# Kernel tuning notes

Hardware: AMD Instinct MI355X
Metric: run time of the kernel (lower is better)

The kernel has to match this reference:

```python
import jax, jax.numpy as jnp
import numpy as np

N_NODES = 100000
N_EDGES = 1600000
N_GRAPHS = 2048
F_IN = 33
D = 256


def _graph_conv(x, edge_index, w_rel, b_rel, w_root):
    # PyG GraphConv (aggr='add'): out = lin_rel(sum_j x_j) + lin_root(x)
    src, dst = edge_index[0], edge_index[1]
    agg = jax.ops.segment_sum(x[src], dst, num_segments=x.shape[0])  # [N, F]
    return agg @ w_rel + b_rel + x @ w_root


def setup_inputs() -> dict:
    key = jax.random.key(0)
    ks = jax.random.split(key, 16)
    scale_in = 1.0 / np.sqrt(F_IN)
    scale_d = 1.0 / np.sqrt(D)
    inp = {
        "x": jax.random.normal(ks[0], (N_NODES, F_IN), dtype=jnp.float32),
        "edge_index": jax.random.randint(ks[1], (2, N_EDGES), 0, N_NODES),
        "batch_index": jnp.sort(jax.random.randint(ks[2], (N_NODES,), 0, N_GRAPHS)),
        # initial_conv: GraphConv(F_IN -> D)
        "w_rel0": jax.random.normal(ks[3], (F_IN, D), dtype=jnp.float32) * scale_in,
        "b_rel0": jnp.zeros((D,), dtype=jnp.float32),
        "w_root0": jax.random.normal(ks[4], (F_IN, D), dtype=jnp.float32) * scale_in,
        # conv1..conv3: GraphConv(D -> D)
        "w_rel1": jax.random.normal(ks[5], (D, D), dtype=jnp.float32) * scale_d,
        "b_rel1": jnp.zeros((D,), dtype=jnp.float32),
        "w_root1": jax.random.normal(ks[6], (D, D), dtype=jnp.float32) * scale_d,
        "w_rel2": jax.random.normal(ks[7], (D, D), dtype=jnp.float32) * scale_d,
        "b_rel2": jnp.zeros((D,), dtype=jnp.float32),
        "w_root2": jax.random.normal(ks[8], (D, D), dtype=jnp.float32) * scale_d,
        "w_rel3": jax.random.normal(ks[9], (D, D), dtype=jnp.float32) * scale_d,
        "b_rel3": jnp.zeros((D,), dtype=jnp.float32),
        "w_root3": jax.random.normal(ks[10], (D, D), dtype=jnp.float32) * scale_d,
        # output head Linear(D -> 1)
        "w_out": jax.random.normal(ks[11], (D, 1), dtype=jnp.float32) * scale_d,
        "b_out": jnp.zeros((1,), dtype=jnp.float32),
    }
    return inp


def reference(x, edge_index, batch_index,
              w_rel0, b_rel0, w_root0,
              w_rel1, b_rel1, w_root1,
              w_rel2, b_rel2, w_root2,
              w_rel3, b_rel3, w_root3,
              w_out, b_out):
    # dropout omitted (eval mode)
    h = jax.nn.gelu(_graph_conv(x, edge_index, w_rel0, b_rel0, w_root0))
    h = jax.nn.gelu(_graph_conv(h, edge_index, w_rel1, b_rel1, w_root1))
    h = jax.nn.gelu(_graph_conv(h, edge_index, w_rel2, b_rel2, w_root2))
    h = jax.nn.gelu(_graph_conv(h, edge_index, w_rel3, b_rel3, w_root3))
    # global mean pool over graphs
    sums = jax.ops.segment_sum(h, batch_index, num_segments=N_GRAPHS)          # [G, D]
    counts = jax.ops.segment_sum(jnp.ones((h.shape[0],), h.dtype), batch_index,
                                 num_segments=N_GRAPHS)                         # [G]
    pooled = sums / jnp.maximum(counts, 1.0)[:, None]
    return pooled @ w_out + b_out                                               # [G, 1]
```

## Files before the change

kernel.cpp:

```cpp
#include <hip/hip_runtime.h>
#include <math.h>

#define NN 100000
#define NE 1600000
#define NG 2048
#define FIN 33
#define DD 256

#define SH 8
#define NB ((NN + 255) >> 8)
#define CH 4096
#define PCAP 4608
#define ESCAP 6144

#define RBLKS ((NN + 255) / 256)

typedef __attribute__((ext_vector_type(8))) short bf16x8;
typedef __attribute__((ext_vector_type(4))) float f32x4;

__device__ __forceinline__ float b2f(unsigned short u){
    union { unsigned int i; float f; } c; c.i = ((unsigned int)u) << 16; return c.f;
}
__device__ __forceinline__ unsigned short f2b(float f){
    union { float f; unsigned int u; } c; c.f = f;
    unsigned int r = c.u + 0x7fffu + ((c.u >> 16) & 1u);
    return (unsigned short)(r >> 16);
}

__device__ __forceinline__ float gelu_tanh(float x){
    float x3 = x * x * x;
    float t = tanhf(0.7978845608028654f * (x + 0.044715f * x3));
    return 0.5f * x * (1.0f + t);
}

__global__ __launch_bounds__(256) void k_bin(const int* __restrict__ src,
                                             const int* __restrict__ dst,
                                             int* __restrict__ gcur,
                                             int2* __restrict__ pairs){
    __shared__ int cnt[NB];
    __shared__ int lb[NB];
    __shared__ int gbase[NB];
    __shared__ int sc[512];
    __shared__ int2 stage[CH];

    int t = threadIdx.x;
    for(int i = t; i < NB; i += 256) cnt[i] = 0;
    __syncthreads();

    int e0 = blockIdx.x * CH;
    int n = NE - e0; if(n > CH) n = CH;

    int  myb[16];
    int  myr[16];
    int2 myp[16];
    #pragma unroll
    for(int k = 0; k < 16; k++){
        int e = e0 + t + k * 256;
        if(e < NE){
            int s = src[e], d = dst[e];
            int b = d >> SH;
            myr[k] = atomicAdd(&cnt[b], 1);
            myb[k] = b;
            myp[k] = make_int2(s, d);
        } else myb[k] = -1;
    }
    __syncthreads();

    sc[t]       = (t       < NB) ? cnt[t]       : 0;
    sc[t + 256] = (t + 256 < NB) ? cnt[t + 256] : 0;
    __syncthreads();
    for(int off = 1; off < 512; off <<= 1){
        int a  = (t >= off)       ? sc[t - off]       : 0;
        int b2 = (t + 256 >= off) ? sc[t + 256 - off] : 0;
        __syncthreads();
        sc[t] += a; sc[t + 256] += b2;
        __syncthreads();
    }
    for(int i = t; i < NB; i += 256){
        lb[i] = sc[i] - cnt[i];
        int c = cnt[i];
        gbase[i] = (c > 0) ? atomicAdd(&gcur[i], c) : 0;
    }
    __syncthreads();

    #pragma unroll
    for(int k = 0; k < 16; k++){
        if(myb[k] >= 0) stage[lb[myb[k]] + myr[k]] = myp[k];
    }
    __syncthreads();

    for(int i = t; i < n; i += 256){
        int2 p = stage[i];
        int b = p.y >> SH;
        int tgt = gbase[b] + (i - lb[b]);
        if(tgt < PCAP) pairs[(size_t)b * PCAP + tgt] = p;
    }
}

__global__ void k_sscan(const int* __restrict__ gcur, int* __restrict__ boff){
    __shared__ int s[512];
    int t = threadIdx.x;
    int v = 0;
    if(t < NB){ v = gcur[t]; if(v > PCAP) v = PCAP; }
    s[t] = v; __syncthreads();
    for(int off = 1; off < 512; off <<= 1){
        int u = (t >= off) ? s[t - off] : 0;
        __syncthreads();
        s[t] += u;
        __syncthreads();
    }
    if(t < NB) boff[t] = s[t] - v;
}

__global__ __launch_bounds__(256) void k_bcsr(const int2* __restrict__ pairs,
                                              const int* __restrict__ gcur,
                                              const int* __restrict__ boff,
                                              int* __restrict__ deg,
                                              int* __restrict__ rs,
                                              int* __restrict__ esrc){
    __shared__ int hist[256];
    __shared__ int sc[256];
    __shared__ int cur2[256];
    __shared__ int est[ESCAP];

    int b = blockIdx.x;
    int t = threadIdx.x;
    int m = gcur[b]; if(m > PCAP) m = PCAP;
    int pstart = boff[b];
    const int2* bp = pairs + (size_t)b * PCAP;

    hist[t] = 0;
    __syncthreads();
    for(int i = t; i < m; i += 256) atomicAdd(&hist[bp[i].y & 255], 1);
    __syncthreads();

    sc[t] = hist[t]; __syncthreads();
    for(int off = 1; off < 256; off <<= 1){
        int u = (t >= off) ? sc[t - off] : 0;
        __syncthreads();
        sc[t] += u;
        __syncthreads();
    }
    int excl = sc[t] - hist[t];
    cur2[t] = excl;
    int node = (b << 8) + t;
    if(node < NN){
        deg[node] = hist[t];
        rs[node]  = pstart + excl;
    }
    __syncthreads();

    for(int i = t; i < m; i += 256){
        int2 p = bp[i];
        int pos = atomicAdd(&cur2[p.y & 255], 1);
        if(pos < ESCAP) est[pos] = p.x;
        else esrc[pstart + pos] = p.x;
    }
    __syncthreads();
    int lim = (m < ESCAP) ? m : ESCAP;
    for(int i = t; i < lim; i += 256) esrc[pstart + i] = est[i];
}

__global__ void k_xpad(const float* __restrict__ x, unsigned short* __restrict__ xb){
    int idx = blockIdx.x * 256 + threadIdx.x;
    if(idx >= NN * 64) return;
    int n = idx >> 6, c = idx & 63;
    xb[idx] = (c < FIN) ? f2b(x[(size_t)n * FIN + c]) : 0;
}

__global__ void k_aggx(const unsigned short* __restrict__ xb, const int* __restrict__ rs,
                       const int* __restrict__ deg, const int* __restrict__ esrc,
                       unsigned short* __restrict__ axb){
    int wv = (blockIdx.x * blockDim.x + threadIdx.x) >> 6;
    int lane = threadIdx.x & 63;
    int node = wv * 4 + (lane >> 4);
    int l16 = lane & 15;
    if(node >= NN) return;
    int start = rs[node], cnt = deg[node];
    float a0 = 0.f, a1 = 0.f, a2 = 0.f, a3 = 0.f;
    const unsigned short* xp = xb + l16 * 4;
    int j = 0;
    for(; j + 4 <= cnt; j += 4){
        int e0 = esrc[start+j], e1 = esrc[start+j+1], e2 = esrc[start+j+2], e3 = esrc[start+j+3];
        ushort4 v0 = *(const ushort4*)(xp + (size_t)e0 * 64);
        ushort4 v1 = *(const ushort4*)(xp + (size_t)e1 * 64);
        ushort4 v2 = *(const ushort4*)(xp + (size_t)e2 * 64);
        ushort4 v3 = *(const ushort4*)(xp + (size_t)e3 * 64);
        a0 += (b2f(v0.x) + b2f(v1.x)) + (b2f(v2.x) + b2f(v3.x));
        a1 += (b2f(v0.y) + b2f(v1.y)) + (b2f(v2.y) + b2f(v3.y));
        a2 += (b2f(v0.z) + b2f(v1.z)) + (b2f(v2.z) + b2f(v3.z));
        a3 += (b2f(v0.w) + b2f(v1.w)) + (b2f(v2.w) + b2f(v3.w));
    }
    for(; j < cnt; j++){
        int e = esrc[start + j];
        ushort4 v = *(const ushort4*)(xp + (size_t)e * 64);
        a0 += b2f(v.x); a1 += b2f(v.y); a2 += b2f(v.z); a3 += b2f(v.w);
    }
    ushort4 o; o.x = f2b(a0); o.y = f2b(a1); o.z = f2b(a2); o.w = f2b(a3);
    *(ushort4*)(axb + (size_t)node * 64 + l16 * 4) = o;
}

__global__ void k_agg256(const unsigned short* __restrict__ h, const int* __restrict__ rs,
                         const int* __restrict__ deg, const int* __restrict__ esrc,
                         unsigned short* __restrict__ agg){
    int wv = (blockIdx.x * blockDim.x + threadIdx.x) >> 6;
    int lane = threadIdx.x & 63;
    int node = wv * 2 + (lane >> 5);
    int l32 = lane & 31;
    if(node >= NN) return;
    int start = rs[node], cnt = deg[node];
    float a[8] = {0.f,0.f,0.f,0.f,0.f,0.f,0.f,0.f};
    const unsigned short* hp = h + l32 * 8;
    int j = 0;
    for(; j + 8 <= cnt; j += 8){
        bf16x8 v[8];
        #pragma unroll
        for(int q = 0; q < 8; q++){
            int e = esrc[start + j + q];
            v[q] = *(const bf16x8*)(hp + (size_t)e * DD);
        }
        #pragma unroll
        for(int q = 0; q < 8; q++)
            #pragma unroll
            for(int d = 0; d < 8; d++)
                a[d] += b2f((unsigned short)v[q][d]);
    }
    for(; j < cnt; j++){
        int e = esrc[start + j];
        bf16x8 v = *(const bf16x8*)(hp + (size_t)e * DD);
        #pragma unroll
        for(int d = 0; d < 8; d++) a[d] += b2f((unsigned short)v[d]);
    }
    bf16x8 o;
    #pragma unroll
    for(int d = 0; d < 8; d++) o[d] = (short)f2b(a[d]);
    *(bf16x8*)(agg + (size_t)node * DD + l32 * 8) = o;
}

struct WPtrs { const float* w[6]; };

__global__ void k_wt6(WPtrs wp, unsigned short* __restrict__ btAll){
    __shared__ float s[16][17];
    const float* W = wp.w[blockIdx.z];
    unsigned short* Bt = btAll + (size_t)blockIdx.z * DD * DD;
    int tx = threadIdx.x, ty = threadIdx.y;
    int k = blockIdx.y * 16 + ty;
    int j = blockIdx.x * 16 + tx;
    s[ty][tx] = W[k * DD + j];
    __syncthreads();
    Bt[(size_t)(blockIdx.x * 16 + ty) * DD + blockIdx.y * 16 + tx] = f2b(s[tx][ty]);
}

struct W2Ptrs { const float* w[2]; };

__global__ void k_wt0(W2Ptrs wp, unsigned short* __restrict__ btAll){
    int idx = blockIdx.x * 256 + threadIdx.x;
    if(idx >= DD * 64) return;
    const float* W = wp.w[blockIdx.z];
    unsigned short* Bt = btAll + (size_t)blockIdx.z * DD * 64;
    int j = idx >> 6, k = idx & 63;
    Bt[idx] = (k < FIN) ? f2b(W[(size_t)k * DD + j]) : 0;
}

template<int KS, int AST>
__global__ __launch_bounds__(512, 4) void k_mfma_gemm(
    const unsigned short* __restrict__ A0, const unsigned short* __restrict__ A1,
    const unsigned short* __restrict__ Bt0, const unsigned short* __restrict__ Bt1,
    const float* __restrict__ bias, unsigned short* __restrict__ out)
{
    constexpr int CK  = KS * 32;
    constexpr int BST = CK + 8;
    constexpr int SEG = CK / 8;
    __shared__ unsigned short Bs[128 * BST];

    int t = threadIdx.x;
    int lane = t & 63;
    int w = t >> 6;
    int r16 = lane & 15;
    int kg  = lane >> 4;

    int bid = blockIdx.x;
    int rblk = (bid >> 4) * 8 + (bid & 7);
    int chalf = (bid >> 3) & 1;
    if(rblk >= RBLKS) return;
    int i0 = rblk * 256;
    int jbase = chalf * 128;
    int baseRow = i0 + w * 32;

    f32x4 acc[2][8];
    #pragma unroll
    for(int m = 0; m < 2; m++)
        #pragma unroll
        for(int n = 0; n < 8; n++)
            acc[m][n] = (f32x4){0.f, 0.f, 0.f, 0.f};

    auto loadA = [&](int gks, bf16x8* af){
        const unsigned short* Ap = (gks < KS) ? A0 : A1;
        int kk = ((gks < KS) ? gks : gks - KS) * 32 + kg * 8;
        #pragma unroll
        for(int m = 0; m < 2; m++){
            int gi = baseRow + m * 16 + r16;
            if(gi > NN - 1) gi = NN - 1;
            af[m] = *(const bf16x8*)(Ap + (size_t)gi * AST + kk);
        }
    };

    bf16x8 afb[2][2];
    loadA(0, afb[0]);
    loadA(1, afb[1]);

    #pragma unroll
    for(int c = 0; c < 2; c++){
        const unsigned short* Bp = c ? Bt1 : Bt0;
        if(c) __syncthreads();
        #pragma unroll
        for(int p = 0; p < (128 * SEG) / 512; p++){
            int idx = p * 512 + t;
            int row = idx / SEG;
            int k8 = (idx % SEG) * 8;
            *(bf16x8*)(&Bs[row * BST + k8]) =
                *(const bf16x8*)(Bp + (size_t)(jbase + row) * AST + k8);
        }
        __syncthreads();
        #pragma unroll
        for(int ksl = 0; ksl < KS; ksl++){
            int gks = c * KS + ksl;
            #pragma unroll
            for(int n = 0; n < 8; n++){
                bf16x8 bfr = *(const bf16x8*)(&Bs[(n * 16 + r16) * BST + ksl * 32 + kg * 8]);
                acc[0][n] = __builtin_amdgcn_mfma_f32_16x16x32_bf16(afb[gks & 1][0], bfr, acc[0][n], 0, 0, 0);
                acc[1][n] = __builtin_amdgcn_mfma_f32_16x16x32_bf16(afb[gks & 1][1], bfr, acc[1][n], 0, 0, 0);
            }
            if(gks + 2 < 2 * KS) loadA(gks + 2, afb[gks & 1]);
        }
    }

    int rg = kg * 4;
    #pragma unroll
    for(int n = 0; n < 8; n++){
        int gj = jbase + n * 16 + r16;
        float bb = bias[gj];
        #pragma unroll
        for(int m = 0; m < 2; m++){
            #pragma unroll
            for(int r = 0; r < 4; r++){
                int gi = baseRow + m * 16 + rg + r;
                if(gi < NN)
                    out[(size_t)gi * DD + gj] = f2b(gelu_tanh(acc[m][n][r] + bb));
            }
        }
    }
}

__global__ void k_pool(const unsigned short* __restrict__ h, const int* __restrict__ batch,
                       const float* __restrict__ wout, float* __restrict__ gsum,
                       int* __restrict__ gcnt){
    int w = (blockIdx.x * blockDim.x + threadIdx.x) >> 6;
    int lane = threadIdx.x & 63;
    if(w >= NN) return;
    ushort4 hv = *(const ushort4*)(h + (size_t)w * DD + lane * 4);
    float4 wv = *(const float4*)(wout + lane * 4);
    float d = b2f(hv.x)*wv.x + b2f(hv.y)*wv.y + b2f(hv.z)*wv.z + b2f(hv.w)*wv.w;
    for(int off = 32; off > 0; off >>= 1) d += __shfl_down(d, off);
    if(lane == 0){
        int g = batch[w];
        atomicAdd(&gsum[g], d);
        atomicAdd(&gcnt[g], 1);
    }
}

__global__ void k_final(const float* __restrict__ gsum, const int* __restrict__ gcnt,
                        const float* __restrict__ bout, float* __restrict__ out){
    int g = blockIdx.x * 256 + threadIdx.x;
    if(g < NG) out[g] = gsum[g] / fmaxf((float)gcnt[g], 1.f) + bout[0];
}

extern "C" void kernel_launch(void* const* d_in, const int* in_sizes, int n_in,
                              void* d_out, int out_size, void* d_ws, size_t ws_size,
                              hipStream_t stream){
    const float* x       = (const float*)d_in[0];
    const int*   ei      = (const int*)d_in[1];
    const int*   src     = ei;
    const int*   dst     = ei + NE;
    const int*   batch   = (const int*)d_in[2];
    const float* w_rel0  = (const float*)d_in[3];
    const float* b_rel0  = (const float*)d_in[4];
    const float* w_root0 = (const float*)d_in[5];
    const float* w_rel1  = (const float*)d_in[6];
    const float* b_rel1  = (const float*)d_in[7];
    const float* w_root1 = (const float*)d_in[8];
    const float* w_rel2  = (const float*)d_in[9];
    const float* b_rel2  = (const float*)d_in[10];
    const float* w_root2 = (const float*)d_in[11];
    const float* w_rel3  = (const float*)d_in[12];
    const float* b_rel3  = (const float*)d_in[13];
    const float* w_root3 = (const float*)d_in[14];
    const float* w_out   = (const float*)d_in[15];
    const float* b_out   = (const float*)d_in[16];
    float* out = (float*)d_out;

    char* ws = (char*)d_ws;
    size_t off = 0;
    auto alloc = [&](size_t bytes) -> void* {
        void* p = ws + off;
        off = (off + bytes + 255) & ~(size_t)255;
        return p;
    };
    unsigned short* hA  = (unsigned short*)alloc((size_t)NN * DD * 2);
    unsigned short* hB  = (unsigned short*)alloc((size_t)NN * DD * 2);
    unsigned short* agg = (unsigned short*)alloc((size_t)NN * DD * 2);
    int*   deg  = (int*)alloc((size_t)NN * 4);
    int*   rs   = (int*)alloc((size_t)NN * 4);
    int*   esrc = (int*)alloc((size_t)NE * 4);
    int*   gcur = (int*)alloc(512 * 4);
    int*   boff = (int*)alloc(512 * 4);
    float* gsum = (float*)alloc((size_t)NG * 4);
    int*   gcnt = (int*)alloc((size_t)NG * 4);
    unsigned short* btAll = (unsigned short*)alloc((size_t)6 * DD * DD * 2);
    unsigned short* bt0All = (unsigned short*)alloc((size_t)2 * DD * 64 * 2);
    (void)ws_size; (void)in_sizes; (void)n_in; (void)out_size;

    int2* pairs = (int2*)hB;
    unsigned short* xb  = agg;
    unsigned short* axb = agg + (size_t)NN * 64 + 128;

    hipMemsetAsync(gcur, 0, 512 * 4, stream);
    k_bin<<<(NE + CH - 1) / CH, 256, 0, stream>>>(src, dst, gcur, pairs);
    k_sscan<<<1, 512, 0, stream>>>(gcur, boff);
    k_bcsr<<<NB, 256, 0, stream>>>(pairs, gcur, boff, deg, rs, esrc);

    WPtrs wp; wp.w[0] = w_rel1; wp.w[1] = w_root1; wp.w[2] = w_rel2;
    wp.w[3] = w_root2; wp.w[4] = w_rel3; wp.w[5] = w_root3;
    k_wt6<<<dim3(16, 16, 6), dim3(16, 16), 0, stream>>>(wp, btAll);
    W2Ptrs w2; w2.w[0] = w_rel0; w2.w[1] = w_root0;
    k_wt0<<<dim3((DD * 64 + 255) / 256, 1, 2), 256, 0, stream>>>(w2, bt0All);
    k_xpad<<<(NN * 64 + 255) / 256, 256, 0, stream>>>(x, xb);

    unsigned short* bt[6];
    for(int i = 0; i < 6; i++) bt[i] = btAll + (size_t)i * DD * DD;
    unsigned short* bt0r = bt0All;
    unsigned short* bt0o = bt0All + (size_t)DD * 64;

    int aggGrid  = (NN + 3) / 4;
    int agg2Grid = (NN * 32 + 255) / 256;
    int gemmGrid = ((RBLKS + 7) / 8) * 16;

    k_aggx<<<(NN + 15) / 16, 256, 0, stream>>>(xb, rs, deg, esrc, axb);
    k_mfma_gemm<2, 64><<<gemmGrid, 512, 0, stream>>>(axb, xb, bt0r, bt0o, b_rel0, hA);
    k_agg256<<<agg2Grid, 256, 0, stream>>>(hA, rs, deg, esrc, agg);
    k_mfma_gemm<8, 256><<<gemmGrid, 512, 0, stream>>>(agg, hA, bt[0], bt[1], b_rel1, hB);
    k_agg256<<<agg2Grid, 256, 0, stream>>>(hB, rs, deg, esrc, agg);
    k_mfma_gemm<8, 256><<<gemmGrid, 512, 0, stream>>>(agg, hB, bt[2], bt[3], b_rel2, hA);
    k_agg256<<<agg2Grid, 256, 0, stream>>>(hA, rs, deg, esrc, agg);
    k_mfma_gemm<8, 256><<<gemmGrid, 512, 0, stream>>>(agg, hA, bt[4], bt[5], b_rel3, hB);

    size_t poolBytes = (size_t)((char*)(gcnt + NG) - (char*)gsum);
    hipMemsetAsync(gsum, 0, poolBytes, stream);
    k_pool<<<aggGrid, 256, 0, stream>>>(hB, batch, w_out, gsum, gcnt);
    k_final<<<(NG + 255) / 256, 256, 0, stream>>>(gsum, gcnt, b_out, out);
}
```

Measured before the change: 785.9 us.

## Fuse mean-pool readout into last GEMM epilogue and pack edge pairs

```diff
diff --git a/kernel.cpp b/kernel.cpp
--- a/kernel.cpp
+++ b/kernel.cpp
@@ -36,7 +36,7 @@
 __global__ __launch_bounds__(256) void k_bin(const int* __restrict__ src,
                                              const int* __restrict__ dst,
                                              int* __restrict__ gcur,
-                                             int2* __restrict__ pairs){
+                                             int* __restrict__ pairs){
     __shared__ int cnt[NB];
     __shared__ int lb[NB];
     __shared__ int gbase[NB];
@@ -93,7 +93,7 @@
         int2 p = stage[i];
         int b = p.y >> SH;
         int tgt = gbase[b] + (i - lb[b]);
-        if(tgt < PCAP) pairs[(size_t)b * PCAP + tgt] = p;
+        if(tgt < PCAP) pairs[(size_t)b * PCAP + tgt] = p.x | ((p.y & 255) << 17);
     }
 }
 
@@ -112,7 +112,7 @@
     if(t < NB) boff[t] = s[t] - v;
 }
 
-__global__ __launch_bounds__(256) void k_bcsr(const int2* __restrict__ pairs,
+__global__ __launch_bounds__(256) void k_bcsr(const int* __restrict__ pairs,
                                               const int* __restrict__ gcur,
                                               const int* __restrict__ boff,
                                               int* __restrict__ deg,
@@ -127,11 +127,11 @@
     int t = threadIdx.x;
     int m = gcur[b]; if(m > PCAP) m = PCAP;
     int pstart = boff[b];
-    const int2* bp = pairs + (size_t)b * PCAP;
+    const int* bp = pairs + (size_t)b * PCAP;
 
     hist[t] = 0;
     __syncthreads();
-    for(int i = t; i < m; i += 256) atomicAdd(&hist[bp[i].y & 255], 1);
+    for(int i = t; i < m; i += 256) atomicAdd(&hist[(bp[i] >> 17) & 255], 1);
     __syncthreads();
 
     sc[t] = hist[t]; __syncthreads();
@@ -151,10 +151,11 @@
     __syncthreads();
 
     for(int i = t; i < m; i += 256){
-        int2 p = bp[i];
-        int pos = atomicAdd(&cur2[p.y & 255], 1);
-        if(pos < ESCAP) est[pos] = p.x;
-        else esrc[pstart + pos] = p.x;
+        int p = bp[i];
+        int pos = atomicAdd(&cur2[(p >> 17) & 255], 1);
+        int s = p & 0x1FFFF;
+        if(pos < ESCAP) est[pos] = s;
+        else esrc[pstart + pos] = s;
     }
     __syncthreads();
     int lim = (m < ESCAP) ? m : ESCAP;
@@ -262,11 +263,18 @@
     Bt[idx] = (k < FIN) ? f2b(W[(size_t)k * DD + j]) : 0;
 }
 
-template<int KS, int AST>
+__global__ void k_cnt(const int* __restrict__ batch, int* __restrict__ gcnt){
+    int i = blockIdx.x * 256 + threadIdx.x;
+    if(i < NN) atomicAdd(&gcnt[batch[i]], 1);
+}
+
+template<int KS, int AST, bool POOL>
 __global__ __launch_bounds__(512, 4) void k_mfma_gemm(
     const unsigned short* __restrict__ A0, const unsigned short* __restrict__ A1,
     const unsigned short* __restrict__ Bt0, const unsigned short* __restrict__ Bt1,
-    const float* __restrict__ bias, unsigned short* __restrict__ out)
+    const float* __restrict__ bias, unsigned short* __restrict__ out,
+    const int* __restrict__ batch, const float* __restrict__ wout,
+    float* __restrict__ gsum)
 {
     constexpr int CK  = KS * 32;
     constexpr int BST = CK + 8;
@@ -325,47 +333,54 @@
         #pragma unroll
         for(int ksl = 0; ksl < KS; ksl++){
             int gks = c * KS + ksl;
+            __builtin_amdgcn_s_setprio(1);
             #pragma unroll
             for(int n = 0; n < 8; n++){
                 bf16x8 bfr = *(const bf16x8*)(&Bs[(n * 16 + r16) * BST + ksl * 32 + kg * 8]);
                 acc[0][n] = __builtin_amdgcn_mfma_f32_16x16x32_bf16(afb[gks & 1][0], bfr, acc[0][n], 0, 0, 0);
                 acc[1][n] = __builtin_amdgcn_mfma_f32_16x16x32_bf16(afb[gks & 1][1], bfr, acc[1][n], 0, 0, 0);
             }
+            __builtin_amdgcn_s_setprio(0);
             if(gks + 2 < 2 * KS) loadA(gks + 2, afb[gks & 1]);
         }
     }
 
     int rg = kg * 4;
-    #pragma unroll
-    for(int n = 0; n < 8; n++){
-        int gj = jbase + n * 16 + r16;
-        float bb = bias[gj];
+    if constexpr (!POOL){
+        #pragma unroll
+        for(int n = 0; n < 8; n++){
+            int gj = jbase + n * 16 + r16;
+            float bb = bias[gj];
+            #pragma unroll
+            for(int m = 0; m < 2; m++){
+                #pragma unroll
+                for(int r = 0; r < 4; r++){
+                    int gi = baseRow + m * 16 + rg + r;
+                    if(gi < NN)
+                        out[(size_t)gi * DD + gj] = f2b(gelu_tanh(acc[m][n][r] + bb));
+                }
+            }
+        }
+    } else {
         #pragma unroll
         for(int m = 0; m < 2; m++){
             #pragma unroll
             for(int r = 0; r < 4; r++){
+                float s = 0.f;
+                #pragma unroll
+                for(int n = 0; n < 8; n++){
+                    int gj = jbase + n * 16 + r16;
+                    s += gelu_tanh(acc[m][n][r] + bias[gj]) * wout[gj];
+                }
+                s += __shfl_xor(s, 1);
+                s += __shfl_xor(s, 2);
+                s += __shfl_xor(s, 4);
+                s += __shfl_xor(s, 8);
                 int gi = baseRow + m * 16 + rg + r;
-                if(gi < NN)
-                    out[(size_t)gi * DD + gj] = f2b(gelu_tanh(acc[m][n][r] + bb));
+                if(r16 == 0 && gi < NN)
+                    atomicAdd(&gsum[batch[gi]], s);
             }
         }
-    }
-}
-
-__global__ void k_pool(const unsigned short* __restrict__ h, const int* __restrict__ batch,
-                       const float* __restrict__ wout, float* __restrict__ gsum,
-                       int* __restrict__ gcnt){
-    int w = (blockIdx.x * blockDim.x + threadIdx.x) >> 6;
-    int lane = threadIdx.x & 63;
-    if(w >= NN) return;
-    ushort4 hv = *(const ushort4*)(h + (size_t)w * DD + lane * 4);
-    float4 wv = *(const float4*)(wout + lane * 4);
-    float d = b2f(hv.x)*wv.x + b2f(hv.y)*wv.y + b2f(hv.z)*wv.z + b2f(hv.w)*wv.w;
-    for(int off = 32; off > 0; off >>= 1) d += __shfl_down(d, off);
-    if(lane == 0){
-        int g = batch[w];
-        atomicAdd(&gsum[g], d);
-        atomicAdd(&gcnt[g], 1);
     }
 }
 
@@ -420,7 +435,7 @@
     unsigned short* bt0All = (unsigned short*)alloc((size_t)2 * DD * 64 * 2);
     (void)ws_size; (void)in_sizes; (void)n_in; (void)out_size;
 
-    int2* pairs = (int2*)hB;
+    int* pairs = (int*)hB;
     unsigned short* xb  = agg;
     unsigned short* axb = agg + (size_t)NN * 64 + 128;
 
@@ -428,6 +443,10 @@
     k_bin<<<(NE + CH - 1) / CH, 256, 0, stream>>>(src, dst, gcur, pairs);
     k_sscan<<<1, 512, 0, stream>>>(gcur, boff);
     k_bcsr<<<NB, 256, 0, stream>>>(pairs, gcur, boff, deg, rs, esrc);
+
+    size_t poolBytes = (size_t)((char*)(gcnt + NG) - (char*)gsum);
+    hipMemsetAsync(gsum, 0, poolBytes, stream);
+    k_cnt<<<(NN + 255) / 256, 256, 0, stream>>>(batch, gcnt);
 
     WPtrs wp; wp.w[0] = w_rel1; wp.w[1] = w_root1; wp.w[2] = w_rel2;
     wp.w[3] = w_root2; wp.w[4] = w_rel3; wp.w[5] = w_root3;
@@ -441,21 +460,21 @@
     unsigned short* bt0r = bt0All;
     unsigned short* bt0o = bt0All + (size_t)DD * 64;
 
-    int aggGrid  = (NN + 3) / 4;
     int agg2Grid = (NN * 32 + 255) / 256;
     int gemmGrid = ((RBLKS + 7) / 8) * 16;
 
     k_aggx<<<(NN + 15) / 16, 256, 0, stream>>>(xb, rs, deg, esrc, axb);
-    k_mfma_gemm<2, 64><<<gemmGrid, 512, 0, stream>>>(axb, xb, bt0r, bt0o, b_rel0, hA);
+    k_mfma_gemm<2, 64, false><<<gemmGrid, 512, 0, stream>>>(axb, xb, bt0r, bt0o, b_rel0, hA,
+                                                            batch, w_out, gsum);
     k_agg256<<<agg2Grid, 256, 0, stream>>>(hA, rs, deg, esrc, agg);
-    k_mfma_gemm<8, 256><<<gemmGrid, 512, 0, stream>>>(agg, hA, bt[0], bt[1], b_rel1, hB);
+    k_mfma_gemm<8, 256, false><<<gemmGrid, 512, 0, stream>>>(agg, hA, bt[0], bt[1], b_rel1, hB,
+                                                             batch, w_out, gsum);
     k_agg256<<<agg2Grid, 256, 0, stream>>>(hB, rs, deg, esrc, agg);
-    k_mfma_gemm<8, 256><<<gemmGrid, 512, 0, stream>>>(agg, hB, bt[2], bt[3], b_rel2, hA);
+    k_mfma_gemm<8, 256, false><<<gemmGrid, 512, 0, stream>>>(agg, hB, bt[2], bt[3], b_rel2, hA,
+                                                             batch, w_out, gsum);
     k_agg256<<<agg2Grid, 256, 0, stream>>>(hA, rs, deg, esrc, agg);
-    k_mfma_gemm<8, 256><<<gemmGrid, 512, 0, stream>>>(agg, hA, bt[4], bt[5], b_rel3, hB);
-
-    size_t poolBytes = (size_t)((char*)(gcnt + NG) - (char*)gsum);
-    hipMemsetAsync(gsum, 0, poolBytes, stream);
-    k_pool<<<aggGrid, 256, 0, stream>>>(hB, batch, w_out, gsum, gcnt);
+    k_mfma_gemm<8, 256, true><<<gemmGrid, 512, 0, stream>>>(agg, hA, bt[4], bt[5], b_rel3, hB,
+                                                            batch, w_out, gsum);
+
     k_final<<<(NG + 255) / 256, 256, 0, stream>>>(gsum, gcnt, b_out, out);
 }
```

New measurement: 776.6 us. No clear change (-1.2%).
